# Performance work log

Measured on AMD Instinct MI355X. Metric: run time of the kernel, lower is better.

The kernel has to match this reference:

```python
import jax, jax.numpy as jnp
import numpy as np

L, H, B = 16, 1024, 4096


def setup_inputs() -> dict:
    key = jax.random.key(0)
    k1, k2, k3, k4 = jax.random.split(key, 4)
    z = jax.random.normal(k1, (B, H), dtype=jnp.float32)
    layer_ids = jax.random.randint(k2, (B,), 0, L)
    # Module initializes weight = identity per layer; add small noise so the
    # transform is non-trivial while staying near the module's init regime.
    eye = jnp.broadcast_to(jnp.eye(H, dtype=jnp.float32), (L, H, H))
    weight = eye + 0.02 * jax.random.normal(k3, (L, H, H), dtype=jnp.float32)
    bias = 0.02 * jax.random.normal(k4, (L, H), dtype=jnp.float32)
    return {"z": z, "layer_ids": layer_ids, "weight": weight, "bias": bias}


def reference(z, layer_ids, weight, bias):
    # Faithful math: out[b] = weight[layer_ids[b]] @ z[b] + bias[layer_ids[b]].
    # Instead of materializing the gathered [B,H,H] weight tensor (as torch.bmm
    # forces), compute all-layer outputs with a grouped GEMM [B,L,H] and select.
    out_all = jnp.einsum('lij,bj->bli', weight, z)  # [B, L, H]
    out = jnp.take_along_axis(out_all, layer_ids[:, None, None], axis=1)[:, 0, :]  # [B, H]
    return out + bias[layer_ids]
```

## Files before the change

kernel.cpp:

```cpp
#include <hip/hip_runtime.h>


#define HDIM 1024
#define LNUM 16
#define BTOT 4096

constexpr int BM = 128, BN = 128, BK = 32;
constexpr int NT = HDIM / BK;

constexpr int LROW = 128;
constexpr int AOFF = 0;
constexpr int BOFF = 16384;
constexpr int BUFSZ = 32768;

typedef __attribute__((ext_vector_type(4))) float floatx4;
typedef __attribute__((ext_vector_type(2))) __fp16 cvt16x2;
typedef __attribute__((ext_vector_type(8))) _Float16 f16x8;
typedef __attribute__((ext_vector_type(2))) unsigned int uintx2;

__global__ void group_kernel(const int* __restrict__ layer_ids,
                             int* __restrict__ perm,
                             int* __restrict__ offsets) {
    __shared__ int cnt[LNUM];
    __shared__ int base[LNUM];
    const int t = threadIdx.x;
    if (t < LNUM) cnt[t] = 0;
    __syncthreads();
    for (int b = t; b < BTOT; b += 256)
        atomicAdd(&cnt[layer_ids[b] & (LNUM - 1)], 1);
    __syncthreads();
    if (t == 0) {
        int acc = 0;
        for (int l = 0; l < LNUM; ++l) {
            base[l] = acc;
            offsets[l] = acc;
            acc += cnt[l];
        }
        offsets[LNUM] = acc;
    }
    __syncthreads();
    if (t < LNUM) cnt[t] = 0;
    __syncthreads();
    for (int b = t; b < BTOT; b += 256) {
        int l = layer_ids[b] & (LNUM - 1);
        int p = base[l] + atomicAdd(&cnt[l], 1);
        perm[p] = b;
    }
}

__device__ __forceinline__ void split4(floatx4 v, uintx2& hw, uintx2& lw) {
    cvt16x2 h01 = __builtin_amdgcn_cvt_pkrtz(v[0], v[1]);
    cvt16x2 h23 = __builtin_amdgcn_cvt_pkrtz(v[2], v[3]);
    cvt16x2 l01 = __builtin_amdgcn_cvt_pkrtz(v[0] - (float)h01[0],
                                             v[1] - (float)h01[1]);
    cvt16x2 l23 = __builtin_amdgcn_cvt_pkrtz(v[2] - (float)h23[0],
                                             v[3] - (float)h23[1]);
    hw[0] = __builtin_bit_cast(unsigned int, h01);
    hw[1] = __builtin_bit_cast(unsigned int, h23);
    lw[0] = __builtin_bit_cast(unsigned int, l01);
    lw[1] = __builtin_bit_cast(unsigned int, l23);
}

__global__ __launch_bounds__(256, 2) void grouped_mfma_kernel(
    const float* __restrict__ z,
    const float* __restrict__ weight,
    const float* __restrict__ bias,
    const int* __restrict__ perm,
    const int* __restrict__ offsets,
    float* __restrict__ out) {

    const int bid  = blockIdx.x;
    const int xcd  = bid & 7;
    const int slot = bid >> 3;
    const int l    = xcd + ((slot >> 8) << 3);
    const int rem  = slot & 255;
    const int my   = rem >> 3;
    const int nx   = rem & 7;

    const int off = offsets[l];
    const int cnt = offsets[l + 1] - off;
    const int m0 = my * BM;
    if (m0 >= cnt) return;
    const int n0 = nx * BN;

    __shared__ __align__(16) unsigned char sm[2][BUFSZ];

    const int tid  = threadIdx.x;
    const int lane = tid & 63;
    const int w    = tid >> 6;
    const int wm   = w & 1;
    const int wn   = w >> 1;

    const int kq  = tid & 7;
    const int rb  = tid >> 3;
    const int swz = (rb & 7) << 1;

    const float* aPtr[4];
    const float* bPtr[4];
#pragma unroll
    for (int p = 0; p < 4; ++p) {
        int gm = m0 + rb + 32 * p;
        if (gm > cnt - 1) gm = cnt - 1;
        aPtr[p] = z + (size_t)perm[off + gm] * HDIM + kq * 4;
        bPtr[p] = weight + (size_t)l * HDIM * HDIM
                         + (size_t)(n0 + rb + 32 * p) * HDIM + kq * 4;
    }
    const int wA_hi = AOFF + rb * LROW + ((kq ^ swz) << 3);
    const int wA_lo = AOFF + rb * LROW + (((8 + kq) ^ swz) << 3);
    const int wB_hi = BOFF + rb * LROW + ((kq ^ swz) << 3);
    const int wB_lo = BOFF + rb * LROW + (((8 + kq) ^ swz) << 3);

    const int lr = lane & 15;
    const int ks = lane >> 4;
    const int rA = wm * 64 + lr;
    const int rB = wn * 64 + lr;
    const int rdA_hi = AOFF + rA * LROW + ((ks ^ (lr & 7)) << 4);
    const int rdA_lo = AOFF + rA * LROW + (((4 + ks) ^ (lr & 7)) << 4);
    const int rdB_hi = BOFF + rB * LROW + ((ks ^ (lr & 7)) << 4);
    const int rdB_lo = BOFF + rB * LROW + (((4 + ks) ^ (lr & 7)) << 4);

    floatx4 acc[4][4] = {};
    floatx4 av[4], bv[4];

    auto loadT = [&](int k0) {
#pragma unroll
        for (int p = 0; p < 4; ++p) {
            av[p] = *(const floatx4*)(aPtr[p] + k0);
            bv[p] = *(const floatx4*)(bPtr[p] + k0);
        }
    };

    auto stageT = [&](unsigned char* buf) {
#pragma unroll
        for (int p = 0; p < 4; ++p) {
            uintx2 hw, lw;
            split4(av[p], hw, lw);
            *(uintx2*)(buf + wA_hi + p * 4096) = hw;
            *(uintx2*)(buf + wA_lo + p * 4096) = lw;
            split4(bv[p], hw, lw);
            *(uintx2*)(buf + wB_hi + p * 4096) = hw;
            *(uintx2*)(buf + wB_lo + p * 4096) = lw;
        }
    };

    auto compute = [&](const unsigned char* buf) {
        f16x8 ah[4], al[4], bh[4], bl[4];
#pragma unroll
        for (int i = 0; i < 4; ++i) {
            ah[i] = *(const f16x8*)(buf + rdA_hi + i * 2048);
            al[i] = *(const f16x8*)(buf + rdA_lo + i * 2048);
            bh[i] = *(const f16x8*)(buf + rdB_hi + i * 2048);
            bl[i] = *(const f16x8*)(buf + rdB_lo + i * 2048);
        }
#pragma unroll
        for (int i = 0; i < 4; ++i)
#pragma unroll
            for (int j = 0; j < 4; ++j) {
                acc[i][j] = __builtin_amdgcn_mfma_f32_16x16x32_f16(
                    ah[i], bh[j], acc[i][j], 0, 0, 0);
                acc[i][j] = __builtin_amdgcn_mfma_f32_16x16x32_f16(
                    ah[i], bl[j], acc[i][j], 0, 0, 0);
                acc[i][j] = __builtin_amdgcn_mfma_f32_16x16x32_f16(
                    al[i], bh[j], acc[i][j], 0, 0, 0);
            }
    };

    loadT(0);
    stageT(sm[0]);
    __syncthreads();

#pragma unroll 1
    for (int t2 = 0; t2 < NT; t2 += 2) {
        loadT((t2 + 1) * BK);
        compute(sm[0]);
        stageT(sm[1]);
        __syncthreads();
        if (t2 + 2 < NT) {
            loadT((t2 + 2) * BK);
            compute(sm[1]);
            stageT(sm[0]);
            __syncthreads();
        } else {
            compute(sm[1]);
        }
    }

    const int colBase = n0 + wn * 64 + lr;
    float bb[4];
#pragma unroll
    for (int j = 0; j < 4; ++j) bb[j] = bias[l * HDIM + colBase + j * 16];

    const int rq = lane >> 4;
#pragma unroll
    for (int i = 0; i < 4; ++i) {
#pragma unroll
        for (int v = 0; v < 4; ++v) {
            int gm = m0 + wm * 64 + i * 16 + rq * 4 + v;
            if (gm < cnt) {
                float* o = out + (size_t)perm[off + gm] * HDIM + colBase;
#pragma unroll
                for (int j = 0; j < 4; ++j) o[j * 16] = acc[i][j][v] + bb[j];
            }
        }
    }
}

extern "C" void kernel_launch(void* const* d_in, const int* in_sizes, int n_in,
                              void* d_out, int out_size, void* d_ws, size_t ws_size,
                              hipStream_t stream) {
    const float* z = nullptr;
    const int* layer_ids = nullptr;
    const float* weight = nullptr;
    const float* bias = nullptr;
    for (int i = 0; i < n_in; ++i) {
        switch (in_sizes[i]) {
            case BTOT * HDIM:        z = (const float*)d_in[i]; break;
            case BTOT:               layer_ids = (const int*)d_in[i]; break;
            case LNUM * HDIM * HDIM: weight = (const float*)d_in[i]; break;
            case LNUM * HDIM:        bias = (const float*)d_in[i]; break;
        }
    }
    float* out = (float*)d_out;

    int* perm = (int*)d_ws;
    int* offsets = perm + BTOT;

    group_kernel<<<1, 256, 0, stream>>>(layer_ids, perm, offsets);

    grouped_mfma_kernel<<<dim3(4096), 256, 0, stream>>>(z, weight, bias, perm,
                                                        offsets, out);
}
```

Measured before the change: 158.0 us.

## Fuse layer grouping into GEMM kernel with per-block ballot scan and persistent M loop

Removes the separate single-block grouping kernel. Each GEMM block now scans layer_ids itself with a bitmask and prefix sum to build its own row permutation tile in shared memory. The M tile shrinks from 128 to 64 rows and occupancy is raised to 3 blocks per CU. The grid is fixed at 1024 blocks, each looping over 8-strided M tiles. This cuts the serial prologue launch and the empty-block waste, but every block now rescans all 4096 ids and rebuilds its permutation on every M iteration. Each weight tile is also reloaded for twice as many M tiles.

```diff
diff --git a/kernel.cpp b/kernel.cpp
--- a/kernel.cpp
+++ b/kernel.cpp
@@ -5,48 +5,19 @@
 #define LNUM 16
 #define BTOT 4096
 
-constexpr int BM = 128, BN = 128, BK = 32;
+constexpr int BM = 64, BN = 128, BK = 32;
 constexpr int NT = HDIM / BK;
+constexpr int MSLOTS = 8;
 
 constexpr int LROW = 128;
 constexpr int AOFF = 0;
-constexpr int BOFF = 16384;
-constexpr int BUFSZ = 32768;
+constexpr int BOFF = 8192;
+constexpr int BUFSZ = 24576;
 
 typedef __attribute__((ext_vector_type(4))) float floatx4;
 typedef __attribute__((ext_vector_type(2))) __fp16 cvt16x2;
 typedef __attribute__((ext_vector_type(8))) _Float16 f16x8;
 typedef __attribute__((ext_vector_type(2))) unsigned int uintx2;
-
-__global__ void group_kernel(const int* __restrict__ layer_ids,
-                             int* __restrict__ perm,
-                             int* __restrict__ offsets) {
-    __shared__ int cnt[LNUM];
-    __shared__ int base[LNUM];
-    const int t = threadIdx.x;
-    if (t < LNUM) cnt[t] = 0;
-    __syncthreads();
-    for (int b = t; b < BTOT; b += 256)
-        atomicAdd(&cnt[layer_ids[b] & (LNUM - 1)], 1);
-    __syncthreads();
-    if (t == 0) {
-        int acc = 0;
-        for (int l = 0; l < LNUM; ++l) {
-            base[l] = acc;
-            offsets[l] = acc;
-            acc += cnt[l];
-        }
-        offsets[LNUM] = acc;
-    }
-    __syncthreads();
-    if (t < LNUM) cnt[t] = 0;
-    __syncthreads();
-    for (int b = t; b < BTOT; b += 256) {
-        int l = layer_ids[b] & (LNUM - 1);
-        int p = base[l] + atomicAdd(&cnt[l], 1);
-        perm[p] = b;
-    }
-}
 
 __device__ __forceinline__ void split4(floatx4 v, uintx2& hw, uintx2& lw) {
     cvt16x2 h01 = __builtin_amdgcn_cvt_pkrtz(v[0], v[1]);
@@ -61,29 +32,21 @@
     lw[1] = __builtin_bit_cast(unsigned int, l23);
 }
 
-__global__ __launch_bounds__(256, 2) void grouped_mfma_kernel(
+__global__ __launch_bounds__(256, 3) void fused_grouped_mfma_kernel(
     const float* __restrict__ z,
+    const int* __restrict__ layer_ids,
     const float* __restrict__ weight,
     const float* __restrict__ bias,
-    const int* __restrict__ perm,
-    const int* __restrict__ offsets,
     float* __restrict__ out) {
 
     const int bid  = blockIdx.x;
     const int xcd  = bid & 7;
     const int slot = bid >> 3;
-    const int l    = xcd + ((slot >> 8) << 3);
-    const int rem  = slot & 255;
+    const int l    = xcd + ((slot >> 6) << 3);
+    const int rem  = slot & 63;
     const int my   = rem >> 3;
     const int nx   = rem & 7;
-
-    const int off = offsets[l];
-    const int cnt = offsets[l + 1] - off;
-    const int m0 = my * BM;
-    if (m0 >= cnt) return;
-    const int n0 = nx * BN;
-
-    __shared__ __align__(16) unsigned char sm[2][BUFSZ];
+    const int n0   = nx * BN;
 
     const int tid  = threadIdx.x;
     const int lane = tid & 63;
@@ -91,20 +54,41 @@
     const int wm   = w & 1;
     const int wn   = w >> 1;
 
+    __shared__ __align__(16) unsigned char sm[2][BUFSZ];
+    __shared__ int permTile[BM];
+    __shared__ int waveSums[4];
+
+    const int4* lid4 = (const int4*)layer_ids;
+    unsigned mask = 0;
+#pragma unroll
+    for (int q = 0; q < 4; ++q) {
+        int4 v = lid4[tid * 4 + q];
+        mask |= (unsigned)(v.x == l) << (4 * q)
+             |  (unsigned)(v.y == l) << (4 * q + 1)
+             |  (unsigned)(v.z == l) << (4 * q + 2)
+             |  (unsigned)(v.w == l) << (4 * q + 3);
+    }
+    const int ct = __popc(mask);
+    int x = ct;
+#pragma unroll
+    for (int o = 1; o < 64; o <<= 1) {
+        int v = __shfl_up(x, o);
+        if (lane >= o) x += v;
+    }
+    if (lane == 63) waveSums[w] = x;
+    __syncthreads();
+    int waveBase = 0, cnt = 0;
+#pragma unroll
+    for (int w2 = 0; w2 < 4; ++w2) {
+        int s = waveSums[w2];
+        if (w2 < w) waveBase += s;
+        cnt += s;
+    }
+    const int et = waveBase + x - ct;
+
     const int kq  = tid & 7;
     const int rb  = tid >> 3;
     const int swz = (rb & 7) << 1;
-
-    const float* aPtr[4];
-    const float* bPtr[4];
-#pragma unroll
-    for (int p = 0; p < 4; ++p) {
-        int gm = m0 + rb + 32 * p;
-        if (gm > cnt - 1) gm = cnt - 1;
-        aPtr[p] = z + (size_t)perm[off + gm] * HDIM + kq * 4;
-        bPtr[p] = weight + (size_t)l * HDIM * HDIM
-                         + (size_t)(n0 + rb + 32 * p) * HDIM + kq * 4;
-    }
     const int wA_hi = AOFF + rb * LROW + ((kq ^ swz) << 3);
     const int wA_lo = AOFF + rb * LROW + (((8 + kq) ^ swz) << 3);
     const int wB_hi = BOFF + rb * LROW + ((kq ^ swz) << 3);
@@ -112,94 +96,126 @@
 
     const int lr = lane & 15;
     const int ks = lane >> 4;
-    const int rA = wm * 64 + lr;
-    const int rB = wn * 64 + lr;
-    const int rdA_hi = AOFF + rA * LROW + ((ks ^ (lr & 7)) << 4);
-    const int rdA_lo = AOFF + rA * LROW + (((4 + ks) ^ (lr & 7)) << 4);
-    const int rdB_hi = BOFF + rB * LROW + ((ks ^ (lr & 7)) << 4);
-    const int rdB_lo = BOFF + rB * LROW + (((4 + ks) ^ (lr & 7)) << 4);
-
-    floatx4 acc[4][4] = {};
-    floatx4 av[4], bv[4];
-
-    auto loadT = [&](int k0) {
-#pragma unroll
-        for (int p = 0; p < 4; ++p) {
-            av[p] = *(const floatx4*)(aPtr[p] + k0);
-            bv[p] = *(const floatx4*)(bPtr[p] + k0);
-        }
-    };
-
-    auto stageT = [&](unsigned char* buf) {
-#pragma unroll
-        for (int p = 0; p < 4; ++p) {
-            uintx2 hw, lw;
-            split4(av[p], hw, lw);
-            *(uintx2*)(buf + wA_hi + p * 4096) = hw;
-            *(uintx2*)(buf + wA_lo + p * 4096) = lw;
-            split4(bv[p], hw, lw);
-            *(uintx2*)(buf + wB_hi + p * 4096) = hw;
-            *(uintx2*)(buf + wB_lo + p * 4096) = lw;
-        }
-    };
-
-    auto compute = [&](const unsigned char* buf) {
-        f16x8 ah[4], al[4], bh[4], bl[4];
-#pragma unroll
-        for (int i = 0; i < 4; ++i) {
-            ah[i] = *(const f16x8*)(buf + rdA_hi + i * 2048);
-            al[i] = *(const f16x8*)(buf + rdA_lo + i * 2048);
-            bh[i] = *(const f16x8*)(buf + rdB_hi + i * 2048);
-            bl[i] = *(const f16x8*)(buf + rdB_lo + i * 2048);
-        }
-#pragma unroll
-        for (int i = 0; i < 4; ++i)
-#pragma unroll
-            for (int j = 0; j < 4; ++j) {
-                acc[i][j] = __builtin_amdgcn_mfma_f32_16x16x32_f16(
-                    ah[i], bh[j], acc[i][j], 0, 0, 0);
-                acc[i][j] = __builtin_amdgcn_mfma_f32_16x16x32_f16(
-                    ah[i], bl[j], acc[i][j], 0, 0, 0);
-                acc[i][j] = __builtin_amdgcn_mfma_f32_16x16x32_f16(
-                    al[i], bh[j], acc[i][j], 0, 0, 0);
-            }
-    };
-
-    loadT(0);
-    stageT(sm[0]);
-    __syncthreads();
-
-#pragma unroll 1
-    for (int t2 = 0; t2 < NT; t2 += 2) {
-        loadT((t2 + 1) * BK);
-        compute(sm[0]);
-        stageT(sm[1]);
-        __syncthreads();
-        if (t2 + 2 < NT) {
-            loadT((t2 + 2) * BK);
-            compute(sm[1]);
-            stageT(sm[0]);
-            __syncthreads();
-        } else {
-            compute(sm[1]);
-        }
-    }
-
+    const int rdA_hi = AOFF + (wm * 32 + lr) * LROW + ((ks ^ (lr & 7)) << 4);
+    const int rdA_lo = AOFF + (wm * 32 + lr) * LROW + (((4 + ks) ^ (lr & 7)) << 4);
+    const int rdB_hi = BOFF + (wn * 64 + lr) * LROW + ((ks ^ (lr & 7)) << 4);
+    const int rdB_lo = BOFF + (wn * 64 + lr) * LROW + (((4 + ks) ^ (lr & 7)) << 4);
+
+    const float* wBase = weight + (size_t)l * HDIM * HDIM;
     const int colBase = n0 + wn * 64 + lr;
     float bb[4];
 #pragma unroll
     for (int j = 0; j < 4; ++j) bb[j] = bias[l * HDIM + colBase + j * 16];
 
-    const int rq = lane >> 4;
-#pragma unroll
-    for (int i = 0; i < 4; ++i) {
-#pragma unroll
-        for (int v = 0; v < 4; ++v) {
-            int gm = m0 + wm * 64 + i * 16 + rq * 4 + v;
-            if (gm < cnt) {
-                float* o = out + (size_t)perm[off + gm] * HDIM + colBase;
-#pragma unroll
-                for (int j = 0; j < 4; ++j) o[j * 16] = acc[i][j][v] + bb[j];
+    for (int m0 = my * BM; m0 < cnt; m0 += MSLOTS * BM) {
+        __syncthreads();
+        {
+            unsigned m2 = mask;
+            int r = et;
+            while (m2) {
+                int p = __ffs(m2) - 1;
+                m2 &= m2 - 1;
+                unsigned rr = (unsigned)(r - m0);
+                if (rr < (unsigned)BM) permTile[rr] = tid * 16 + p;
+                ++r;
+            }
+        }
+        __syncthreads();
+
+        const float* aPtr[2];
+        const float* bPtr[4];
+#pragma unroll
+        for (int p = 0; p < 2; ++p) {
+            int gm = rb + 32 * p;
+            if (gm > cnt - 1 - m0) gm = cnt - 1 - m0;
+            aPtr[p] = z + (size_t)permTile[gm] * HDIM + kq * 4;
+        }
+#pragma unroll
+        for (int p = 0; p < 4; ++p)
+            bPtr[p] = wBase + (size_t)(n0 + rb + 32 * p) * HDIM + kq * 4;
+
+        floatx4 acc[2][4] = {};
+        floatx4 av[2], bv[4];
+
+        auto loadT = [&](int k0) {
+#pragma unroll
+            for (int p = 0; p < 2; ++p) av[p] = *(const floatx4*)(aPtr[p] + k0);
+#pragma unroll
+            for (int p = 0; p < 4; ++p) bv[p] = *(const floatx4*)(bPtr[p] + k0);
+        };
+
+        auto stageT = [&](unsigned char* buf) {
+            uintx2 hw, lw;
+#pragma unroll
+            for (int p = 0; p < 2; ++p) {
+                split4(av[p], hw, lw);
+                *(uintx2*)(buf + wA_hi + p * 4096) = hw;
+                *(uintx2*)(buf + wA_lo + p * 4096) = lw;
+            }
+#pragma unroll
+            for (int p = 0; p < 4; ++p) {
+                split4(bv[p], hw, lw);
+                *(uintx2*)(buf + wB_hi + p * 4096) = hw;
+                *(uintx2*)(buf + wB_lo + p * 4096) = lw;
+            }
+        };
+
+        auto compute = [&](const unsigned char* buf) {
+            f16x8 ah[2], al[2], bh[4], bl[4];
+#pragma unroll
+            for (int i = 0; i < 2; ++i) {
+                ah[i] = *(const f16x8*)(buf + rdA_hi + i * 2048);
+                al[i] = *(const f16x8*)(buf + rdA_lo + i * 2048);
+            }
+#pragma unroll
+            for (int j = 0; j < 4; ++j) {
+                bh[j] = *(const f16x8*)(buf + rdB_hi + j * 2048);
+                bl[j] = *(const f16x8*)(buf + rdB_lo + j * 2048);
+            }
+#pragma unroll
+            for (int i = 0; i < 2; ++i)
+#pragma unroll
+                for (int j = 0; j < 4; ++j) {
+                    acc[i][j] = __builtin_amdgcn_mfma_f32_16x16x32_f16(
+                        ah[i], bh[j], acc[i][j], 0, 0, 0);
+                    acc[i][j] = __builtin_amdgcn_mfma_f32_16x16x32_f16(
+                        ah[i], bl[j], acc[i][j], 0, 0, 0);
+                    acc[i][j] = __builtin_amdgcn_mfma_f32_16x16x32_f16(
+                        al[i], bh[j], acc[i][j], 0, 0, 0);
+                }
+        };
+
+        loadT(0);
+        stageT(sm[0]);
+        __syncthreads();
+
+#pragma unroll 1
+        for (int t2 = 0; t2 < NT; t2 += 2) {
+            loadT((t2 + 1) * BK);
+            compute(sm[0]);
+            stageT(sm[1]);
+            __syncthreads();
+            if (t2 + 2 < NT) {
+                loadT((t2 + 2) * BK);
+                compute(sm[1]);
+                stageT(sm[0]);
+                __syncthreads();
+            } else {
+                compute(sm[1]);
+            }
+        }
+
+        const int rq = lane >> 4;
+#pragma unroll
+        for (int i = 0; i < 2; ++i) {
+#pragma unroll
+            for (int v = 0; v < 4; ++v) {
+                int gm = wm * 32 + i * 16 + rq * 4 + v;
+                if (m0 + gm < cnt) {
+                    float* o = out + (size_t)permTile[gm] * HDIM + colBase;
+#pragma unroll
+                    for (int j = 0; j < 4; ++j) o[j * 16] = acc[i][j][v] + bb[j];
+                }
             }
         }
     }
@@ -222,11 +238,6 @@
     }
     float* out = (float*)d_out;
 
-    int* perm = (int*)d_ws;
-    int* offsets = perm + BTOT;
-
-    group_kernel<<<1, 256, 0, stream>>>(layer_ids, perm, offsets);
-
-    grouped_mfma_kernel<<<dim3(4096), 256, 0, stream>>>(z, weight, bias, perm,
-                                                        offsets, out);
+    fused_grouped_mfma_kernel<<<dim3(1024), 256, 0, stream>>>(
+        z, layer_ids, weight, bias, out);
 }
```

After: 146.1 us. 7.5% less time.
